# Performance work log

Hardware: AMD Instinct MI355X
Metric: run time of the kernel (lower is better)

## Reference

```python
import jax, jax.numpy as jnp
import numpy as np

B, F, D = 4096, 32, 32
LAYER_SIZE = [128, 128]


def setup_inputs() -> dict:
    key = jax.random.key(0)
    k1, k2, k3 = jax.random.split(key, 3)
    inputs = jax.random.normal(k1, (B, F, D), dtype=jnp.float32)
    # CIN filters: shape [1, field_nums[0]*field_nums[i], field_nums[i+1]]
    field_nums = [F] + LAYER_SIZE
    filter_0 = (jax.random.normal(k2, (1, field_nums[0] * field_nums[0], field_nums[1]), dtype=jnp.float32) * 0.05)
    filter_1 = (jax.random.normal(k3, (1, field_nums[0] * field_nums[1], field_nums[2]), dtype=jnp.float32) * 0.05)
    return {"inputs": inputs, "filter_0": filter_0, "filter_1": filter_1}


def _cin_forward(inputs, filters):
    x0 = inputs          # [B, F, D] -- hidden_nn_layers[0]
    prev = inputs        # hidden_nn_layers[-1]
    outs = []
    for W in filters:    # W: [1, F*M, N]
        # outer product over field dims: [B, F, M, D]
        z = jnp.einsum('bhd,bmd->bhmd', x0, prev)
        b, h, m, d = z.shape
        z = z.reshape(b, h * m, d)                 # [B, F*M, D]
        # 1x1 conv over the F*M axis == contraction with W[0]: [F*M, N]
        cur = jnp.einsum('bpd,pn->bnd', z, W[0])   # [B, N, D]
        cur = jax.nn.relu(cur)
        prev = cur
        outs.append(cur)
    result = jnp.concatenate(outs, axis=1)         # [B, sum(layer_size), D]
    return jnp.sum(result, axis=-1)                # [B, sum(layer_size)]


def reference(inputs, filter_0, filter_1):
    return _cin_forward(inputs, (filter_0, filter_1))
```

## Files before the change

kernel.cpp:

```cpp
#include <hip/hip_runtime.h>


typedef _Float16 half_t;
typedef _Float16 half4v __attribute__((ext_vector_type(4)));
typedef _Float16 half8 __attribute__((ext_vector_type(8)));
typedef float f32x16 __attribute__((ext_vector_type(16)));

__global__ void prep_w_kernel(const float* __restrict__ W0,
                              const float* __restrict__ W1,
                              half_t* __restrict__ Wp0,
                              half_t* __restrict__ Wp1) {
  int gid = blockIdx.x * 256 + threadIdx.x;
  int n = gid & 127;
  int tg = (gid >> 7) & 1;
  int s = gid >> 8;
  const float* W;
  half_t* Wp;
  int M, sl;
  if (s < 64) { W = W0; Wp = Wp0; M = 32; sl = s; }
  else        { W = W1; Wp = Wp1; M = 128; sl = s - 64; }
  int h = sl & 31, mc = sl >> 5;
  int kbase = h * M + mc * 16 + tg * 8;
  half8 v;
#pragma unroll
  for (int j = 0; j < 8; ++j) v[j] = (half_t)W[(size_t)(kbase + j) * 128 + n];
  *(half8*)(Wp + ((size_t)(sl * 2 + tg) * 128 + n) * 8) = v;
}

__device__ __forceinline__ int pswz(int row, int m) {
  return row * 128 + (((m >> 3) ^ (row & 15)) << 3) + (m & 7);
}

__device__ __forceinline__ f32x16 mfma3216(half8 a, half8 b, f32x16 c) {
  return __builtin_amdgcn_mfma_f32_32x32x16_f16(a, b, c, 0, 0, 0);
}

template <int MC, bool L1>
__device__ __forceinline__ void layer_loop(const half_t* __restrict__ Wp,
                                           const half_t* __restrict__ psrc,
                                           const half_t* __restrict__ xQw,
                                           int woff0, int woff1, int rowb,
                                           int l31, int hi, f32x16 acc[4][2]) {
  half8 B0a0 = *(const half8*)(Wp + 0 * 2048 + woff0);
  half8 B0a1 = *(const half8*)(Wp + 0 * 2048 + woff1);
  half8 B1a0 = *(const half8*)(Wp + 1 * 2048 + woff0);
  half8 B1a1 = *(const half8*)(Wp + 1 * 2048 + woff1);
  half8 B0b0 = *(const half8*)(Wp + 2 * 2048 + woff0);
  half8 B0b1 = *(const half8*)(Wp + 2 * 2048 + woff1);
  half8 B1b0 = *(const half8*)(Wp + 3 * 2048 + woff0);
  half8 B1b1 = *(const half8*)(Wp + 3 * 2048 + woff1);
  half8 xqa = *(const half8*)(xQw);
  half8 xqb = *(const half8*)(xQw + 256);

  half8 P[4];
#pragma unroll
  for (int rt = 0; rt < 4; ++rt)
    P[rt] = L1 ? *(const half8*)&psrc[(rowb + rt * 32 + l31) * 40 + hi * 8]
               : *(const half8*)&psrc[pswz(rowb + rt * 32 + l31, hi * 8)];

#pragma unroll 1
  for (int mc = 0; mc < MC; ++mc) {
#pragma unroll 1
    for (int p = 0; p < 8; ++p) {
      const int g0 = mc * 16 + 2 * p;
#pragma unroll
      for (int rt = 0; rt < 4; ++rt) {
        half8 Af = P[rt] * xqa[rt * 2 + 0];
        acc[rt][0] = mfma3216(Af, B0a0, acc[rt][0]);
        acc[rt][1] = mfma3216(Af, B0a1, acc[rt][1]);
      }
#pragma unroll
      for (int rt = 0; rt < 4; ++rt) {
        half8 Af = P[rt] * xqa[rt * 2 + 1];
        acc[rt][0] = mfma3216(Af, B1a0, acc[rt][0]);
        acc[rt][1] = mfma3216(Af, B1a1, acc[rt][1]);
      }
      {
        const int sn = (2 * (g0 + 2)) & (MC * 32 - 1);
        B0a0 = *(const half8*)(Wp + (size_t)sn * 2048 + woff0);
        B0a1 = *(const half8*)(Wp + (size_t)sn * 2048 + woff1);
        B1a0 = *(const half8*)(Wp + (size_t)(sn + 1) * 2048 + woff0);
        B1a1 = *(const half8*)(Wp + (size_t)(sn + 1) * 2048 + woff1);
        xqa = *(const half8*)(xQw + ((2 * p + 2) & 15) * 256);
      }
#pragma unroll
      for (int rt = 0; rt < 4; ++rt) {
        half8 Af = P[rt] * xqb[rt * 2 + 0];
        acc[rt][0] = mfma3216(Af, B0b0, acc[rt][0]);
        acc[rt][1] = mfma3216(Af, B0b1, acc[rt][1]);
      }
#pragma unroll
      for (int rt = 0; rt < 4; ++rt) {
        half8 Af = P[rt] * xqb[rt * 2 + 1];
        acc[rt][0] = mfma3216(Af, B1b0, acc[rt][0]);
        acc[rt][1] = mfma3216(Af, B1b1, acc[rt][1]);
      }
      {
        const int sn = (2 * (g0 + 3)) & (MC * 32 - 1);
        B0b0 = *(const half8*)(Wp + (size_t)sn * 2048 + woff0);
        B0b1 = *(const half8*)(Wp + (size_t)sn * 2048 + woff1);
        B1b0 = *(const half8*)(Wp + (size_t)(sn + 1) * 2048 + woff0);
        B1b1 = *(const half8*)(Wp + (size_t)(sn + 1) * 2048 + woff1);
        xqb = *(const half8*)(xQw + ((2 * p + 3) & 15) * 256);
      }
    }
    if (mc + 1 < MC) {
      const int mn = (mc + 1) * 16;
#pragma unroll
      for (int rt = 0; rt < 4; ++rt)
        P[rt] = L1 ? *(const half8*)&psrc[(rowb + rt * 32 + l31) * 40 + mn +
                                          hi * 8]
                   : *(const half8*)&psrc[pswz(rowb + rt * 32 + l31,
                                               mn + hi * 8)];
    }
  }
}

__global__ __launch_bounds__(256, 2) void cin_fused_kernel(
    const float* __restrict__ x0,
    const half_t* __restrict__ Wp0,
    const half_t* __restrict__ Wp1,
    float* __restrict__ out) {
  __shared__ half_t xQ[2 * 16 * 32 * 8];
  __shared__ half_t prevT[8 * 32 * 128];
  half_t* xT = prevT;

  const int tid = threadIdx.x;
  const int b0 = blockIdx.x * 8;

  const float4* x4 = (const float4*)(x0 + (size_t)b0 * 1024);
#pragma unroll
  for (int r = 0; r < 8; ++r) {
    int q = r * 256 + tid;
    float4 v = x4[q];
    int e4 = q * 4;
    int bi = e4 >> 10, h = (e4 >> 5) & 31, d0 = e4 & 31;
    half4v hv = {(half_t)v.x, (half_t)v.y, (half_t)v.z, (half_t)v.w};
    const int quad = bi >> 2, rtl = bi & 3;
#pragma unroll
    for (int j = 0; j < 4; ++j) {
      xQ[quad * 4096 + (h >> 1) * 256 + (d0 + j) * 8 + rtl * 2 + (h & 1)] =
          hv[j];
      xT[(bi * 32 + d0 + j) * 40 + h] = hv[j];
    }
  }
  __syncthreads();

  const int lane = tid & 63;
  const int l31 = lane & 31;
  const int hi = lane >> 5;
  const int wave = tid >> 6;
  const int wr = wave >> 1;
  const int wc = wave & 1;

  const int woff0 = hi * 1024 + (wc * 64 + l31) * 8;
  const int woff1 = hi * 1024 + (wc * 64 + 32 + l31) * 8;
  const int rowb = wr * 128;
  const half_t* xQw = xQ + wr * 4096 + l31 * 8;

  f32x16 acc[4][2];
#pragma unroll
  for (int rt = 0; rt < 4; ++rt)
#pragma unroll
    for (int ct = 0; ct < 2; ++ct)
#pragma unroll
      for (int r = 0; r < 16; ++r) acc[rt][ct][r] = 0.f;

  layer_loop<2, true>(Wp0, xT, xQw, woff0, woff1, rowb, l31, hi, acc);

  __syncthreads();

#pragma unroll
  for (int rt = 0; rt < 4; ++rt) {
#pragma unroll
    for (int ct = 0; ct < 2; ++ct) {
      float s = 0.f;
#pragma unroll
      for (int r = 0; r < 16; ++r) {
        float v = acc[rt][ct][r];
        v = v > 0.f ? v : 0.f;
        s += v;
        int d = (r & 3) + ((r >> 2) << 3) + hi * 4;
        prevT[pswz(rowb + rt * 32 + d, wc * 64 + ct * 32 + l31)] = (half_t)v;
        acc[rt][ct][r] = 0.f;
      }
      s += __shfl_down(s, 32);
      if (lane < 32)
        out[(size_t)(b0 + wr * 4 + rt) * 256 + wc * 64 + ct * 32 + lane] = s;
    }
  }
  __syncthreads();

  layer_loop<8, false>(Wp1, prevT, xQw, woff0, woff1, rowb, l31, hi, acc);

#pragma unroll
  for (int rt = 0; rt < 4; ++rt) {
#pragma unroll
    for (int ct = 0; ct < 2; ++ct) {
      float s = 0.f;
#pragma unroll
      for (int r = 0; r < 16; ++r) {
        float v = acc[rt][ct][r];
        s += v > 0.f ? v : 0.f;
      }
      s += __shfl_down(s, 32);
      if (lane < 32)
        out[(size_t)(b0 + wr * 4 + rt) * 256 + 128 + wc * 64 + ct * 32 +
            lane] = s;
    }
  }
}

extern "C" void kernel_launch(void* const* d_in, const int* in_sizes, int n_in,
                              void* d_out, int out_size, void* d_ws,
                              size_t ws_size, hipStream_t stream) {
  const float* x0 = (const float*)d_in[0];
  const float* w0 = (const float*)d_in[1];
  const float* w1 = (const float*)d_in[2];
  float* out = (float*)d_out;
  char* ws = (char*)d_ws;

  half_t* Wp0 = (half_t*)(ws);
  half_t* Wp1 = (half_t*)(ws + 64 * 2048 * 2);

  hipLaunchKernelGGL(prep_w_kernel, dim3(320), dim3(256), 0, stream, w0, w1,
                     Wp0, Wp1);
  hipLaunchKernelGGL(cin_fused_kernel, dim3(512), dim3(256), 0, stream, x0,
                     Wp0, Wp1, out);
}
```

Baseline: 191.8 us.

## Double-buffer P fragments, prefetch weights early, and swizzle block order

Splits the inner mc loop into ping-pong passes so the next chunk's P fragments load from LDS mid-pass (at p==5) into a second register set, instead of stalling after the pass. The first-layer weight fragments are issued before the x staging loop, and the second-layer weight fragments before the barrier and epilogue, so global latency overlaps other work. Block indices are remapped with a stride-64 swizzle to change how batches spread across CUs. This costs extra VGPRs for the Pn buffer, which may pressure occupancy at launch_bounds(256,2).

```diff
diff --git a/kernel.cpp b/kernel.cpp
--- a/kernel.cpp
+++ b/kernel.cpp
@@ -35,84 +35,87 @@
   return __builtin_amdgcn_mfma_f32_32x32x16_f16(a, b, c, 0, 0, 0);
 }
 
+template <bool L1>
+__device__ __forceinline__ half8 p_read(const half_t* __restrict__ psrc,
+                                        int row, int m) {
+  return L1 ? *(const half8*)&psrc[row * 40 + m]
+            : *(const half8*)&psrc[pswz(row, m)];
+}
+
 template <int MC, bool L1>
-__device__ __forceinline__ void layer_loop(const half_t* __restrict__ Wp,
-                                           const half_t* __restrict__ psrc,
-                                           const half_t* __restrict__ xQw,
-                                           int woff0, int woff1, int rowb,
-                                           int l31, int hi, f32x16 acc[4][2]) {
-  half8 B0a0 = *(const half8*)(Wp + 0 * 2048 + woff0);
-  half8 B0a1 = *(const half8*)(Wp + 0 * 2048 + woff1);
-  half8 B1a0 = *(const half8*)(Wp + 1 * 2048 + woff0);
-  half8 B1a1 = *(const half8*)(Wp + 1 * 2048 + woff1);
-  half8 B0b0 = *(const half8*)(Wp + 2 * 2048 + woff0);
-  half8 B0b1 = *(const half8*)(Wp + 2 * 2048 + woff1);
-  half8 B1b0 = *(const half8*)(Wp + 3 * 2048 + woff0);
-  half8 B1b1 = *(const half8*)(Wp + 3 * 2048 + woff1);
-  half8 xqa = *(const half8*)(xQw);
-  half8 xqb = *(const half8*)(xQw + 256);
-
-  half8 P[4];
-#pragma unroll
-  for (int rt = 0; rt < 4; ++rt)
-    P[rt] = L1 ? *(const half8*)&psrc[(rowb + rt * 32 + l31) * 40 + hi * 8]
-               : *(const half8*)&psrc[pswz(rowb + rt * 32 + l31, hi * 8)];
-
+__device__ __forceinline__ void mc_pass(
+    const half_t* __restrict__ Wp, const half_t* __restrict__ psrc,
+    const half_t* __restrict__ xQw, int woff0, int woff1, int rowb, int l31,
+    int hi, f32x16 acc[4][2], half8& B0a0, half8& B0a1, half8& B1a0,
+    half8& B1a1, half8& B0b0, half8& B0b1, half8& B1b0, half8& B1b1,
+    half8& xqa, half8& xqb, half8 Pc[4], half8 Pn[4], int mc, bool hasNext) {
 #pragma unroll 1
-  for (int mc = 0; mc < MC; ++mc) {
+  for (int p = 0; p < 8; ++p) {
+    const int g0 = mc * 16 + 2 * p;
+#pragma unroll
+    for (int rt = 0; rt < 4; ++rt) {
+      half8 Af = Pc[rt] * xqa[rt * 2 + 0];
+      acc[rt][0] = mfma3216(Af, B0a0, acc[rt][0]);
+      acc[rt][1] = mfma3216(Af, B0a1, acc[rt][1]);
+    }
+#pragma unroll
+    for (int rt = 0; rt < 4; ++rt) {
+      half8 Af = Pc[rt] * xqa[rt * 2 + 1];
+      acc[rt][0] = mfma3216(Af, B1a0, acc[rt][0]);
+      acc[rt][1] = mfma3216(Af, B1a1, acc[rt][1]);
+    }
+    {
+      const int sn = (2 * (g0 + 2)) & (MC * 32 - 1);
+      B0a0 = *(const half8*)(Wp + (size_t)sn * 2048 + woff0);
+      B0a1 = *(const half8*)(Wp + (size_t)sn * 2048 + woff1);
+      B1a0 = *(const half8*)(Wp + (size_t)(sn + 1) * 2048 + woff0);
+      B1a1 = *(const half8*)(Wp + (size_t)(sn + 1) * 2048 + woff1);
+      xqa = *(const half8*)(xQw + ((2 * p + 2) & 15) * 256);
+    }
+#pragma unroll
+    for (int rt = 0; rt < 4; ++rt) {
+      half8 Af = Pc[rt] * xqb[rt * 2 + 0];
+      acc[rt][0] = mfma3216(Af, B0b0, acc[rt][0]);
+      acc[rt][1] = mfma3216(Af, B0b1, acc[rt][1]);
+    }
+#pragma unroll
+    for (int rt = 0; rt < 4; ++rt) {
+      half8 Af = Pc[rt] * xqb[rt * 2 + 1];
+      acc[rt][0] = mfma3216(Af, B1b0, acc[rt][0]);
+      acc[rt][1] = mfma3216(Af, B1b1, acc[rt][1]);
+    }
+    {
+      const int sn = (2 * (g0 + 3)) & (MC * 32 - 1);
+      B0b0 = *(const half8*)(Wp + (size_t)sn * 2048 + woff0);
+      B0b1 = *(const half8*)(Wp + (size_t)sn * 2048 + woff1);
+      B1b0 = *(const half8*)(Wp + (size_t)(sn + 1) * 2048 + woff0);
+      B1b1 = *(const half8*)(Wp + (size_t)(sn + 1) * 2048 + woff1);
+      xqb = *(const half8*)(xQw + ((2 * p + 3) & 15) * 256);
+    }
+    if (p == 5 && hasNext) {
+      const int mn = (mc + 1) * 16 + hi * 8;
+#pragma unroll
+      for (int rt = 0; rt < 4; ++rt)
+        Pn[rt] = p_read<L1>(psrc, rowb + rt * 32 + l31, mn);
+    }
+  }
+}
+
+template <int MC, bool L1>
+__device__ __forceinline__ void layer_loop(
+    const half_t* __restrict__ Wp, const half_t* __restrict__ psrc,
+    const half_t* __restrict__ xQw, int woff0, int woff1, int rowb, int l31,
+    int hi, f32x16 acc[4][2], half8& B0a0, half8& B0a1, half8& B1a0,
+    half8& B1a1, half8& B0b0, half8& B0b1, half8& B1b0, half8& B1b1,
+    half8& xqa, half8& xqb, half8 P[4], half8 Pn[4]) {
 #pragma unroll 1
-    for (int p = 0; p < 8; ++p) {
-      const int g0 = mc * 16 + 2 * p;
-#pragma unroll
-      for (int rt = 0; rt < 4; ++rt) {
-        half8 Af = P[rt] * xqa[rt * 2 + 0];
-        acc[rt][0] = mfma3216(Af, B0a0, acc[rt][0]);
-        acc[rt][1] = mfma3216(Af, B0a1, acc[rt][1]);
-      }
-#pragma unroll
-      for (int rt = 0; rt < 4; ++rt) {
-        half8 Af = P[rt] * xqa[rt * 2 + 1];
-        acc[rt][0] = mfma3216(Af, B1a0, acc[rt][0]);
-        acc[rt][1] = mfma3216(Af, B1a1, acc[rt][1]);
-      }
-      {
-        const int sn = (2 * (g0 + 2)) & (MC * 32 - 1);
-        B0a0 = *(const half8*)(Wp + (size_t)sn * 2048 + woff0);
-        B0a1 = *(const half8*)(Wp + (size_t)sn * 2048 + woff1);
-        B1a0 = *(const half8*)(Wp + (size_t)(sn + 1) * 2048 + woff0);
-        B1a1 = *(const half8*)(Wp + (size_t)(sn + 1) * 2048 + woff1);
-        xqa = *(const half8*)(xQw + ((2 * p + 2) & 15) * 256);
-      }
-#pragma unroll
-      for (int rt = 0; rt < 4; ++rt) {
-        half8 Af = P[rt] * xqb[rt * 2 + 0];
-        acc[rt][0] = mfma3216(Af, B0b0, acc[rt][0]);
-        acc[rt][1] = mfma3216(Af, B0b1, acc[rt][1]);
-      }
-#pragma unroll
-      for (int rt = 0; rt < 4; ++rt) {
-        half8 Af = P[rt] * xqb[rt * 2 + 1];
-        acc[rt][0] = mfma3216(Af, B1b0, acc[rt][0]);
-        acc[rt][1] = mfma3216(Af, B1b1, acc[rt][1]);
-      }
-      {
-        const int sn = (2 * (g0 + 3)) & (MC * 32 - 1);
-        B0b0 = *(const half8*)(Wp + (size_t)sn * 2048 + woff0);
-        B0b1 = *(const half8*)(Wp + (size_t)sn * 2048 + woff1);
-        B1b0 = *(const half8*)(Wp + (size_t)(sn + 1) * 2048 + woff0);
-        B1b1 = *(const half8*)(Wp + (size_t)(sn + 1) * 2048 + woff1);
-        xqb = *(const half8*)(xQw + ((2 * p + 3) & 15) * 256);
-      }
-    }
-    if (mc + 1 < MC) {
-      const int mn = (mc + 1) * 16;
-#pragma unroll
-      for (int rt = 0; rt < 4; ++rt)
-        P[rt] = L1 ? *(const half8*)&psrc[(rowb + rt * 32 + l31) * 40 + mn +
-                                          hi * 8]
-                   : *(const half8*)&psrc[pswz(rowb + rt * 32 + l31,
-                                               mn + hi * 8)];
-    }
+  for (int mcp = 0; mcp < MC / 2; ++mcp) {
+    mc_pass<MC, L1>(Wp, psrc, xQw, woff0, woff1, rowb, l31, hi, acc, B0a0,
+                    B0a1, B1a0, B1a1, B0b0, B0b1, B1b0, B1b1, xqa, xqb, P, Pn,
+                    2 * mcp, true);
+    mc_pass<MC, L1>(Wp, psrc, xQw, woff0, woff1, rowb, l31, hi, acc, B0a0,
+                    B0a1, B1a0, B1a1, B0b0, B0b1, B1b0, B1b1, xqa, xqb, Pn, P,
+                    2 * mcp + 1, 2 * mcp + 2 < MC);
   }
 }
 
@@ -126,7 +129,29 @@
   half_t* xT = prevT;
 
   const int tid = threadIdx.x;
-  const int b0 = blockIdx.x * 8;
+  const int bsw = (blockIdx.x & 7) * 64 + (blockIdx.x >> 3);
+  const int b0 = bsw * 8;
+
+  const int lane = tid & 63;
+  const int l31 = lane & 31;
+  const int hi = lane >> 5;
+  const int wave = tid >> 6;
+  const int wr = wave >> 1;
+  const int wc = wave & 1;
+
+  const int woff0 = hi * 1024 + (wc * 64 + l31) * 8;
+  const int woff1 = hi * 1024 + (wc * 64 + 32 + l31) * 8;
+  const int rowb = wr * 128;
+  const half_t* xQw = xQ + wr * 4096 + l31 * 8;
+
+  half8 B0a0 = *(const half8*)(Wp0 + 0 * 2048 + woff0);
+  half8 B0a1 = *(const half8*)(Wp0 + 0 * 2048 + woff1);
+  half8 B1a0 = *(const half8*)(Wp0 + 1 * 2048 + woff0);
+  half8 B1a1 = *(const half8*)(Wp0 + 1 * 2048 + woff1);
+  half8 B0b0 = *(const half8*)(Wp0 + 2 * 2048 + woff0);
+  half8 B0b1 = *(const half8*)(Wp0 + 2 * 2048 + woff1);
+  half8 B1b0 = *(const half8*)(Wp0 + 3 * 2048 + woff0);
+  half8 B1b1 = *(const half8*)(Wp0 + 3 * 2048 + woff1);
 
   const float4* x4 = (const float4*)(x0 + (size_t)b0 * 1024);
 #pragma unroll
@@ -146,17 +171,12 @@
   }
   __syncthreads();
 
-  const int lane = tid & 63;
-  const int l31 = lane & 31;
-  const int hi = lane >> 5;
-  const int wave = tid >> 6;
-  const int wr = wave >> 1;
-  const int wc = wave & 1;
-
-  const int woff0 = hi * 1024 + (wc * 64 + l31) * 8;
-  const int woff1 = hi * 1024 + (wc * 64 + 32 + l31) * 8;
-  const int rowb = wr * 128;
-  const half_t* xQw = xQ + wr * 4096 + l31 * 8;
+  half8 xqa = *(const half8*)(xQw);
+  half8 xqb = *(const half8*)(xQw + 256);
+  half8 P[4], Pn[4];
+#pragma unroll
+  for (int rt = 0; rt < 4; ++rt)
+    P[rt] = p_read<true>(xT, rowb + rt * 32 + l31, hi * 8);
 
   f32x16 acc[4][2];
 #pragma unroll
@@ -166,7 +186,20 @@
 #pragma unroll
       for (int r = 0; r < 16; ++r) acc[rt][ct][r] = 0.f;
 
-  layer_loop<2, true>(Wp0, xT, xQw, woff0, woff1, rowb, l31, hi, acc);
+  layer_loop<2, true>(Wp0, xT, xQw, woff0, woff1, rowb, l31, hi, acc, B0a0,
+                      B0a1, B1a0, B1a1, B0b0, B0b1, B1b0, B1b1, xqa, xqb, P,
+                      Pn);
+
+  B0a0 = *(const half8*)(Wp1 + 0 * 2048 + woff0);
+  B0a1 = *(const half8*)(Wp1 + 0 * 2048 + woff1);
+  B1a0 = *(const half8*)(Wp1 + 1 * 2048 + woff0);
+  B1a1 = *(const half8*)(Wp1 + 1 * 2048 + woff1);
+  B0b0 = *(const half8*)(Wp1 + 2 * 2048 + woff0);
+  B0b1 = *(const half8*)(Wp1 + 2 * 2048 + woff1);
+  B1b0 = *(const half8*)(Wp1 + 3 * 2048 + woff0);
+  B1b1 = *(const half8*)(Wp1 + 3 * 2048 + woff1);
+  xqa = *(const half8*)(xQw);
+  xqb = *(const half8*)(xQw + 256);
 
   __syncthreads();
 
@@ -191,7 +224,13 @@
   }
   __syncthreads();
 
-  layer_loop<8, false>(Wp1, prevT, xQw, woff0, woff1, rowb, l31, hi, acc);
+#pragma unroll
+  for (int rt = 0; rt < 4; ++rt)
+    P[rt] = p_read<false>(prevT, rowb + rt * 32 + l31, hi * 8);
+
+  layer_loop<8, false>(Wp1, prevT, xQw, woff0, woff1, rowb, l31, hi, acc,
+                       B0a0, B0a1, B1a0, B1a1, B0b0, B0b1, B1b0, B1b1, xqa,
+                       xqb, P, Pn);
 
 #pragma unroll
   for (int rt = 0; rt < 4; ++rt) {
```

Measured after the change: 199.6 us. 1.04x slower.
